# Kernel tuning notes

Measured on AMD Instinct MI355X. Metric: run time of the kernel, lower is better.

The kernel has to match this reference:

```python
import jax, jax.numpy as jnp
import numpy as np

# Neighbor offsets (dy, dx) for kernels j=0..7. Each torch conv with a
# [-1 at neighbor, +1 at center] 3x3 kernel and padding=1 equals
# x - shift(x, offset) with zero-padded borders.
_OFFSETS = [(0, -1), (1, -1), (1, 0), (1, 1), (0, 1), (-1, 1), (-1, 0), (-1, -1)]
_EPS = 1e-5


def setup_inputs() -> dict:
    key = jax.random.key(0)
    x = jax.random.normal(key, (32, 1, 1024, 1024), dtype=jnp.float32)
    return {"x": x}


def _ltpe_forward(x):
    B, C, H, W = x.shape
    xp = jnp.pad(x, ((0, 0), (0, 0), (1, 1), (1, 1)))  # zero border, matches conv padding=1
    out = jnp.zeros_like(x)
    for j, (dy, dx) in enumerate(_OFFSETS):
        nb = jax.lax.dynamic_slice(xp, (0, 0, 1 + dy, 1 + dx), (B, C, H, W))
        diff = x - nb                      # conv output for kernel j
        out = out + ((diff + 1.0) * 0.5) * (float(2 ** j) / 255.0)
    # InstanceNorm2d(1): normalize over (H, W) per sample/channel, no affine,
    # biased variance, eps=1e-5.
    mean = jnp.mean(out, axis=(2, 3), keepdims=True)
    var = jnp.var(out, axis=(2, 3), keepdims=True)
    return (out - mean) * jax.lax.rsqrt(var + _EPS)


def reference(x):
    return _ltpe_forward(x)
```

## Files before the change

kernel.cpp:

```cpp
#include <hip/hip_runtime.h>


#define HH 1024
#define WW 1024
#define NIMG 32
#define NBLK 64
#define ROWS_PER_BLK (HH / NBLK)
#define TPB 256

typedef float vfloat4 __attribute__((ext_vector_type(4)));

__device__ __forceinline__ void compute_y(const float* up, const float* mid,
                                          const float* dn, float* y) {
    const float w0 = 1.f / 255.f,  w1 = 2.f / 255.f,  w2 = 4.f / 255.f,
                w3 = 8.f / 255.f,  w4 = 16.f / 255.f, w5 = 32.f / 255.f,
                w6 = 64.f / 255.f, w7 = 128.f / 255.f;
#pragma unroll
    for (int k = 0; k < 4; ++k) {
        float s = w0 * mid[k] + w4 * mid[k + 2]
                + w1 * dn[k]  + w2 * dn[k + 1] + w3 * dn[k + 2]
                + w7 * up[k]  + w6 * up[k + 1] + w5 * up[k + 2];
        y[k] = mid[k + 1] - s;
    }
}

__device__ __forceinline__ void load_row(const float* __restrict__ row, int c,
                                         float* buf) {
    const vfloat4 v = reinterpret_cast<const vfloat4*>(row)[c];
    buf[0] = (c > 0) ? row[4 * c - 1] : 0.f;
    buf[1] = v.x; buf[2] = v.y; buf[3] = v.z; buf[4] = v.w;
    buf[5] = (c < TPB - 1) ? row[4 * c + 4] : 0.f;
}

__device__ __forceinline__ void zero_row(float* buf) {
#pragma unroll
    for (int k = 0; k < 6; ++k) buf[k] = 0.f;
}

__global__ __launch_bounds__(TPB) void ltpe_stats(const float* __restrict__ x,
                                                  float* __restrict__ partials) {
    const int img = blockIdx.x / NBLK;
    const int blk = blockIdx.x % NBLK;
    const int c = threadIdx.x;
    const float* base = x + (size_t)img * HH * WW;
    const int r0 = blk * ROWS_PER_BLK;

    float up[6], mid[6], dn[6];
    if (r0 > 0) load_row(base + (size_t)(r0 - 1) * WW, c, up); else zero_row(up);
    load_row(base + (size_t)r0 * WW, c, mid);

    float s = 0.f, ss = 0.f;
    for (int i = 0; i < ROWS_PER_BLK; ++i) {
        const int r = r0 + i;
        if (r + 1 < HH) load_row(base + (size_t)(r + 1) * WW, c, dn);
        else zero_row(dn);
        float y[4];
        compute_y(up, mid, dn, y);
#pragma unroll
        for (int k = 0; k < 4; ++k) { s += y[k]; ss = fmaf(y[k], y[k], ss); }
#pragma unroll
        for (int k = 0; k < 6; ++k) { up[k] = mid[k]; mid[k] = dn[k]; }
    }

#pragma unroll
    for (int off = 32; off > 0; off >>= 1) {
        s += __shfl_down(s, off);
        ss += __shfl_down(ss, off);
    }
    __shared__ float sh[8];
    const int wave = threadIdx.x >> 6;
    const int lane = threadIdx.x & 63;
    if (lane == 0) { sh[wave] = s; sh[4 + wave] = ss; }
    __syncthreads();
    if (threadIdx.x == 0) {
        float S = sh[0] + sh[1] + sh[2] + sh[3];
        float SS = sh[4] + sh[5] + sh[6] + sh[7];
        partials[img * NBLK + blk] = S;
        partials[NIMG * NBLK + img * NBLK + blk] = SS;
    }
}

__global__ __launch_bounds__(TPB) void ltpe_norm(const float* __restrict__ x,
                                                 const float* __restrict__ partials,
                                                 float* __restrict__ out) {
    const int img = blockIdx.x / NBLK;
    const int blk = blockIdx.x % NBLK;
    const int c = threadIdx.x;

    __shared__ float sh_stats[2];
    if (threadIdx.x < 64) {
        const int lane = threadIdx.x;
        double S = (double)partials[img * NBLK + lane];
        double SS = (double)partials[NIMG * NBLK + img * NBLK + lane];
#pragma unroll
        for (int off = 32; off > 0; off >>= 1) {
            S += __shfl_down(S, off);
            SS += __shfl_down(SS, off);
        }
        if (lane == 0) {
            const double N = (double)HH * (double)WW;
            const double mean = S / N;
            const double var = SS / N - mean * mean;
            sh_stats[0] = (float)mean;
            sh_stats[1] = (float)(1.0 / sqrt(var + 4e-5));
        }
    }
    __syncthreads();
    const float mean = sh_stats[0];
    const float scale = sh_stats[1];

    const float* base = x + (size_t)img * HH * WW;
    float* obase = out + (size_t)img * HH * WW;
    const int r0 = blk * ROWS_PER_BLK;

    float up[6], mid[6], dn[6];
    if (r0 > 0) load_row(base + (size_t)(r0 - 1) * WW, c, up); else zero_row(up);
    load_row(base + (size_t)r0 * WW, c, mid);

    for (int i = 0; i < ROWS_PER_BLK; ++i) {
        const int r = r0 + i;
        if (r + 1 < HH) load_row(base + (size_t)(r + 1) * WW, c, dn);
        else zero_row(dn);
        float y[4];
        compute_y(up, mid, dn, y);
        vfloat4 o;
        o.x = (y[0] - mean) * scale;
        o.y = (y[1] - mean) * scale;
        o.z = (y[2] - mean) * scale;
        o.w = (y[3] - mean) * scale;
        vfloat4* op = reinterpret_cast<vfloat4*>(obase + (size_t)r * WW) + c;
        __builtin_nontemporal_store(o, op);
#pragma unroll
        for (int k = 0; k < 6; ++k) { up[k] = mid[k]; mid[k] = dn[k]; }
    }
}

extern "C" void kernel_launch(void* const* d_in, const int* in_sizes, int n_in,
                              void* d_out, int out_size, void* d_ws, size_t ws_size,
                              hipStream_t stream) {
    const float* x = (const float*)d_in[0];
    float* out = (float*)d_out;
    float* partials = (float*)d_ws;

    ltpe_stats<<<NIMG * NBLK, TPB, 0, stream>>>(x, partials);
    ltpe_norm<<<NIMG * NBLK, TPB, 0, stream>>>(x, partials, out);
}
```

Baseline: 72.21 us.

## Fuse stats and normalize passes into one cooperative kernel with grid sync

Merges the statistics kernel and the normalization kernel into a single cooperative launch separated by a grid-wide barrier, and halves the blocks per image to 32 so all 1024 blocks can be co-resident. This removes one kernel launch and lets the second pass reread input that may still sit in cache. In exchange it adds grid-sync cost and fewer blocks per image, so each thread runs a longer serial row loop.

```diff
diff --git a/kernel.cpp b/kernel.cpp
--- a/kernel.cpp
+++ b/kernel.cpp
@@ -1,14 +1,17 @@
 #include <hip/hip_runtime.h>
+#include <hip/hip_cooperative_groups.h>
 
 
 #define HH 1024
 #define WW 1024
 #define NIMG 32
-#define NBLK 64
+#define NBLK 32
 #define ROWS_PER_BLK (HH / NBLK)
 #define TPB 256
 
 typedef float vfloat4 __attribute__((ext_vector_type(4)));
+
+namespace cg = cooperative_groups;
 
 __device__ __forceinline__ void compute_y(const float* up, const float* mid,
                                           const float* dn, float* y) {
@@ -37,61 +40,60 @@
     for (int k = 0; k < 6; ++k) buf[k] = 0.f;
 }
 
-__global__ __launch_bounds__(TPB) void ltpe_stats(const float* __restrict__ x,
-                                                  float* __restrict__ partials) {
+__global__ __launch_bounds__(TPB) void ltpe_fused(const float* __restrict__ x,
+                                                  float* __restrict__ partials,
+                                                  float* __restrict__ out) {
     const int img = blockIdx.x / NBLK;
     const int blk = blockIdx.x % NBLK;
     const int c = threadIdx.x;
     const float* base = x + (size_t)img * HH * WW;
     const int r0 = blk * ROWS_PER_BLK;
 
-    float up[6], mid[6], dn[6];
-    if (r0 > 0) load_row(base + (size_t)(r0 - 1) * WW, c, up); else zero_row(up);
-    load_row(base + (size_t)r0 * WW, c, mid);
+    {
+        float up[6], mid[6], dn[6];
+        if (r0 > 0) load_row(base + (size_t)(r0 - 1) * WW, c, up); else zero_row(up);
+        load_row(base + (size_t)r0 * WW, c, mid);
 
-    float s = 0.f, ss = 0.f;
-    for (int i = 0; i < ROWS_PER_BLK; ++i) {
-        const int r = r0 + i;
-        if (r + 1 < HH) load_row(base + (size_t)(r + 1) * WW, c, dn);
-        else zero_row(dn);
-        float y[4];
-        compute_y(up, mid, dn, y);
+        float s = 0.f, ss = 0.f;
+        for (int i = 0; i < ROWS_PER_BLK; ++i) {
+            const int r = r0 + i;
+            if (r + 1 < HH) load_row(base + (size_t)(r + 1) * WW, c, dn);
+            else zero_row(dn);
+            float y[4];
+            compute_y(up, mid, dn, y);
 #pragma unroll
-        for (int k = 0; k < 4; ++k) { s += y[k]; ss = fmaf(y[k], y[k], ss); }
+            for (int k = 0; k < 4; ++k) { s += y[k]; ss = fmaf(y[k], y[k], ss); }
 #pragma unroll
-        for (int k = 0; k < 6; ++k) { up[k] = mid[k]; mid[k] = dn[k]; }
+            for (int k = 0; k < 6; ++k) { up[k] = mid[k]; mid[k] = dn[k]; }
+        }
+
+#pragma unroll
+        for (int off = 32; off > 0; off >>= 1) {
+            s += __shfl_down(s, off);
+            ss += __shfl_down(ss, off);
+        }
+        __shared__ float sh[8];
+        const int wave = threadIdx.x >> 6;
+        const int lane = threadIdx.x & 63;
+        if (lane == 0) { sh[wave] = s; sh[4 + wave] = ss; }
+        __syncthreads();
+        if (threadIdx.x == 0) {
+            partials[img * NBLK + blk] = sh[0] + sh[1] + sh[2] + sh[3];
+            partials[NIMG * NBLK + img * NBLK + blk] = sh[4] + sh[5] + sh[6] + sh[7];
+        }
     }
 
-#pragma unroll
-    for (int off = 32; off > 0; off >>= 1) {
-        s += __shfl_down(s, off);
-        ss += __shfl_down(ss, off);
-    }
-    __shared__ float sh[8];
-    const int wave = threadIdx.x >> 6;
-    const int lane = threadIdx.x & 63;
-    if (lane == 0) { sh[wave] = s; sh[4 + wave] = ss; }
-    __syncthreads();
-    if (threadIdx.x == 0) {
-        float S = sh[0] + sh[1] + sh[2] + sh[3];
-        float SS = sh[4] + sh[5] + sh[6] + sh[7];
-        partials[img * NBLK + blk] = S;
-        partials[NIMG * NBLK + img * NBLK + blk] = SS;
-    }
-}
-
-__global__ __launch_bounds__(TPB) void ltpe_norm(const float* __restrict__ x,
-                                                 const float* __restrict__ partials,
-                                                 float* __restrict__ out) {
-    const int img = blockIdx.x / NBLK;
-    const int blk = blockIdx.x % NBLK;
-    const int c = threadIdx.x;
+    __threadfence();
+    cg::this_grid().sync();
 
     __shared__ float sh_stats[2];
     if (threadIdx.x < 64) {
         const int lane = threadIdx.x;
-        double S = (double)partials[img * NBLK + lane];
-        double SS = (double)partials[NIMG * NBLK + img * NBLK + lane];
+        double S = 0.0, SS = 0.0;
+        if (lane < NBLK) {
+            S = (double)partials[img * NBLK + lane];
+            SS = (double)partials[NIMG * NBLK + img * NBLK + lane];
+        }
 #pragma unroll
         for (int off = 32; off > 0; off >>= 1) {
             S += __shfl_down(S, off);
@@ -109,10 +111,7 @@
     const float mean = sh_stats[0];
     const float scale = sh_stats[1];
 
-    const float* base = x + (size_t)img * HH * WW;
     float* obase = out + (size_t)img * HH * WW;
-    const int r0 = blk * ROWS_PER_BLK;
-
     float up[6], mid[6], dn[6];
     if (r0 > 0) load_row(base + (size_t)(r0 - 1) * WW, c, up); else zero_row(up);
     load_row(base + (size_t)r0 * WW, c, mid);
@@ -142,6 +141,7 @@
     float* out = (float*)d_out;
     float* partials = (float*)d_ws;
 
-    ltpe_stats<<<NIMG * NBLK, TPB, 0, stream>>>(x, partials);
-    ltpe_norm<<<NIMG * NBLK, TPB, 0, stream>>>(x, partials, out);
+    void* args[] = {(void*)&x, (void*)&partials, (void*)&out};
+    hipLaunchCooperativeKernel((const void*)ltpe_fused, dim3(NIMG * NBLK),
+                               dim3(TPB), args, 0, stream);
 }
```

Measured after the change: 196.6 us. 2.72x slower.
